# Optimization experiments

Hardware: AMD Instinct MI355X
Metric: run time of the kernel (lower is better)

Reference implementation:

```python
import jax, jax.numpy as jnp
import numpy as np

B, N, DEG = 64, 512, 16        # graphs, nodes per graph, avg degree
C, HID = 10, 128               # input feat dim (== num_classes quirk), hidden
E = B * N * DEG                # total edges (fixed; pooling masks edges)


def _gcn(x, W, b, src, dst, emask, n):
    # PyG GCNConv: add self-loops, symmetric norm D^-1/2 (A+I) D^-1/2 (XW) + b
    h = x @ W
    deg = jax.ops.segment_sum(emask, dst, num_segments=n) + 1.0  # +1 self-loop
    dinv = jax.lax.rsqrt(deg)
    norm = dinv[src] * dinv[dst] * emask
    agg = jax.ops.segment_sum(h[src] * norm[:, None], dst, num_segments=n)
    return agg + h * (dinv * dinv)[:, None] + b  # self-loop term + bias


def _sag_pool(x, src, dst, emask, Wp, bp, n_per):
    # SAGPooling: score = tanh(GCN(x)); per-graph top-k (ratio=0.5); x' = x[perm]*score
    n = x.shape[0]
    score = jnp.tanh(_gcn(x, Wp, bp, src, dst, emask, n)[:, 0])
    k = n_per // 2
    vals, idx = jax.lax.top_k(score.reshape(B, n_per), k)  # [B,k]
    perm = (idx + (jnp.arange(B) * n_per)[:, None]).reshape(-1)
    xk = x[perm] * vals.reshape(-1)[:, None]
    # relabel edges; drop edges touching removed nodes via mask (fixed E)
    mapping = jnp.full((n,), -1, jnp.int32).at[perm].set(
        jnp.arange(B * k, dtype=jnp.int32))
    ns, nd = mapping[src], mapping[dst]
    nmask = emask * ((ns >= 0) & (nd >= 0)).astype(emask.dtype)
    return xk, jnp.maximum(ns, 0), jnp.maximum(nd, 0), nmask, k


def _readout(x, k):
    # global max pool || global mean pool (all kept nodes are real, no padding)
    xg = x.reshape(B, k, -1)
    return jnp.concatenate([xg.max(axis=1), xg.mean(axis=1)], axis=1)


def setup_inputs() -> dict:
    key = jax.random.key(0)
    ks = jax.random.split(key, 16)
    x = jax.random.normal(ks[0], (B * N, C), jnp.float32)
    off = jnp.repeat(jnp.arange(B, dtype=jnp.int32) * N, N * DEG)
    src = jax.random.randint(ks[1], (E,), 0, N, jnp.int32) + off
    dst = jax.random.randint(ks[2], (E,), 0, N, jnp.int32) + off
    p = lambda k, s: jax.random.normal(k, s, jnp.float32) * 0.05
    return {
        "x": x, "src": src, "dst": dst,
        "W1": p(ks[3], (C, HID)), "b1": jnp.zeros((HID,), jnp.float32),
        "W2": p(ks[4], (HID, HID)), "b2": jnp.zeros((HID,), jnp.float32),
        "W3": p(ks[5], (HID, HID)), "b3": jnp.zeros((HID,), jnp.float32),
        "Wp": p(ks[6], (HID, 1)), "bp": jnp.zeros((1,), jnp.float32),
        "L1W": p(ks[7], (2 * HID, HID)), "L1b": jnp.zeros((HID,), jnp.float32),
        "L2W": p(ks[8], (HID, HID // 2)), "L2b": jnp.zeros((HID // 2,), jnp.float32),
    }


def reference(x, src, dst, W1, b1, W2, b2, W3, b3, Wp, bp, L1W, L1b, L2W, L2b):
    emask = jnp.ones((E,), jnp.float32)
    h = jax.nn.relu(_gcn(x, W1, b1, src, dst, emask, B * N))
    h, src, dst, emask, k = _sag_pool(h, src, dst, emask, Wp, bp, N)
    x1 = _readout(h, k)
    h = jax.nn.relu(_gcn(h, W2, b2, src, dst, emask, B * k))
    h, src, dst, emask, k = _sag_pool(h, src, dst, emask, Wp, bp, k)
    x2 = _readout(h, k)
    h = jax.nn.relu(_gcn(h, W3, b3, src, dst, emask, B * k))
    h, src, dst, emask, k = _sag_pool(h, src, dst, emask, Wp, bp, k)
    x3 = _readout(h, k)
    z = x1 + x2 + x3
    z = jax.nn.relu(z @ L1W + L1b)
    # dropout inactive in eval mode
    z = jax.nn.relu(z @ L2W + L2b)
    return jax.nn.log_softmax(z, axis=1)
```

## Files before the change

### kernel.cpp

```cpp
#include <hip/hip_runtime.h>
#include <math.h>

#define BGR 64
#define N0 512
#define E_TOT (BGR*N0*16)
#define EPG 8192
#define EIT 16
#define HID 128
#define LOFF2 32768
#define LOFF3 49152

#define HSW(r,l) (((r)<<3) | (((l)+(r))&7))

__device__ __forceinline__ void bitonic_sort(float* sv, int* si, float v, int idx,
                                             int t, int nper, bool act){
  for (int kk = 2; kk <= nper; kk <<= 1){
    for (int jj = kk >> 1; jj > 0; jj >>= 1){
      if (jj >= 64){
        if (act){ sv[t] = v; si[t] = idx; }
        __syncthreads();
        if (act){
          int p = t ^ jj;
          float pv = sv[p]; int pi = si[p];
          bool amLower = (t & jj) == 0;
          bool dirDesc = (t & kk) == 0;
          bool betterMine = (v > pv) || (v == pv && idx < pi);
          if ((amLower == dirDesc) != betterMine){ v = pv; idx = pi; }
        }
        __syncthreads();
      } else if (act){
        float pv = __shfl_xor(v, jj);
        int   pi = __shfl_xor(idx, jj);
        bool amLower = (t & jj) == 0;
        bool dirDesc = (t & kk) == 0;
        bool betterMine = (v > pv) || (v == pv && idx < pi);
        if ((amLower == dirDesc) != betterMine){ v = pv; idx = pi; }
      }
    }
  }
  if (act){ sv[t] = v; si[t] = idx; }
  __syncthreads();
}

__device__ __forceinline__ void relabel_pre(
    int2* __restrict__ edges, int2* __restrict__ csr, const int* si,
    int* map_, int* sb, int* cur, float* dl, int* wsum,
    int* __restrict__ rowptr, int* __restrict__ cnt, float* __restrict__ dinv,
    const int2* epre,
    int t, int nper, int k, int gbase, int gbnew, int ebase, int loff){
  if (t < nper) map_[t] = -1;
  if (t < k) sb[t] = 0;
  __syncthreads();
  if (t < k) map_[si[t]] = t;
  __syncthreads();
  int2 ebuf[8];
  #pragma unroll
  for (int it = 0; it < 8; it++){
    int2 e = epre[it];
    int2 ne = make_int2(-1, 0);
    if (e.x >= 0){
      int ns = map_[e.x - gbase], nd = map_[e.y - gbase];
      if (ns >= 0 && nd >= 0){
        ne = make_int2(gbnew + ns, gbnew + nd);
        atomicAdd(&sb[nd], 1);
      }
    }
    ebuf[it] = ne;
    edges[ebase + it*1024 + t] = ne;
  }
  __syncthreads();
  int vdeg = (t < k) ? sb[t] : 0;
  int lane = t & 63, wid = t >> 6;
  int x = vdeg;
  #pragma unroll
  for (int off = 1; off < 64; off <<= 1){
    int y = __shfl_up(x, off);
    if (lane >= off) x += y;
  }
  if (t < k && lane == 63) wsum[wid] = x;
  __syncthreads();
  if (t < k){
    int prefix = 0;
    #pragma unroll
    for (int wj = 0; wj < 4; wj++) prefix += (wj < wid) ? wsum[wj] : 0;
    int excl = x + prefix - vdeg;
    rowptr[loff + gbnew + t] = ebase + excl;
    cnt[loff + gbnew + t] = vdeg;
    cur[t] = excl;
    float dv = rsqrtf((float)vdeg + 1.f);
    dl[t] = dv;
    dinv[loff + gbnew + t] = dv;
  }
  __syncthreads();
  #pragma unroll
  for (int it = 0; it < 8; it++){
    int2 e = ebuf[it];
    if (e.x >= 0){
      int sl = e.x - gbnew, dc = e.y - gbnew;
      int pos = atomicAdd(&cur[dc], 1);
      csr[ebase + pos] = make_int2(e.x, __float_as_int(dl[sl]*dl[dc]));
    }
  }
  __syncthreads();
}

__global__ __launch_bounds__(512) void k_topo0(
    const int* __restrict__ s0, const int* __restrict__ d0,
    int2* __restrict__ edges, int* __restrict__ cnt, int* __restrict__ rowptr,
    float* __restrict__ dinv, int2* __restrict__ csr){
  __shared__ int   deg[512];
  __shared__ int   cur[512];
  __shared__ float dl[512];
  __shared__ int   wsum[8];
  int g = (blockIdx.x & 7)*8 + (blockIdx.x >> 3);
  int t = threadIdx.x;
  int gbase = g*N0, ebase = g*EPG;
  deg[t] = 0;
  __syncthreads();
  int2 ebuf[EIT];
  #pragma unroll
  for (int it = 0; it < EIT; it++){
    int i = ebase + it*512 + t;
    int2 e = make_int2(s0[i], d0[i]);
    ebuf[it] = e;
    edges[i] = e;
    atomicAdd(&deg[e.y - gbase], 1);
  }
  __syncthreads();
  int vdeg = deg[t];
  int lane = t & 63, wid = t >> 6;
  int x = vdeg;
  #pragma unroll
  for (int off = 1; off < 64; off <<= 1){
    int y = __shfl_up(x, off);
    if (lane >= off) x += y;
  }
  if (lane == 63) wsum[wid] = x;
  __syncthreads();
  int prefix = 0;
  #pragma unroll
  for (int wj = 0; wj < 8; wj++) prefix += (wj < wid) ? wsum[wj] : 0;
  int excl = x + prefix - vdeg;
  rowptr[gbase + t] = ebase + excl;
  cnt[gbase + t] = vdeg;
  cur[t] = excl;
  float dv = rsqrtf((float)vdeg + 1.f);
  dl[t] = dv;
  dinv[gbase + t] = dv;
  __syncthreads();
  #pragma unroll
  for (int it = 0; it < EIT; it++){
    int2 e = ebuf[it];
    int sl = e.x - gbase, dc = e.y - gbase;
    int pos = atomicAdd(&cur[dc], 1);
    csr[ebase + pos] = make_int2(e.x, __float_as_int(dl[sl]*dl[dc]));
  }
}

__global__ __launch_bounds__(512) void k_l1_fused(
    const float* __restrict__ x, const float* __restrict__ W1,
    const int2* __restrict__ csr, const int* __restrict__ rowptr,
    const int* __restrict__ cnt, const float* __restrict__ dinv,
    const float* __restrict__ b1, const float* __restrict__ Wp,
    float4* __restrict__ gout4, float* __restrict__ hp_part){
  extern __shared__ float hl[];
  int b = blockIdx.x;
  int xcd = b & 7, idx = b >> 3;
  int graph = xcd*8 + (idx >> 3);
  int sub = idx & 7;
  int qf = sub >> 1, half = sub & 1;
  int t = threadIdx.x;
  int gbase = graph*N0;
  int fp = t & 31;
  int f = qf*32 + fp;
  float wcol[10];
  #pragma unroll
  for (int k = 0; k < 10; k++) wcol[k] = W1[k*HID + f];
  for (int n = t >> 5; n < N0; n += 16){
    const float* xr = x + (gbase + n)*10;
    float acc = 0.f;
    #pragma unroll
    for (int k = 0; k < 10; k++) acc += xr[k]*wcol[k];
    hl[n*32 + ((((fp>>2)+n)&7)<<2) + (fp&3)] = acc;
  }
  __syncthreads();
  const float4* hl4 = (const float4*)hl;
  int l = t & 7, grp = t >> 3;
  float4 bb = ((const float4*)b1)[qf*8 + l];
  float4 wp = ((const float4*)Wp)[qf*8 + l];
  int n0 = half*256;
  for (int nl = n0 + grp; nl < n0 + 256; nl += 64){
    int node = gbase + nl;
    int start = rowptr[node], c = cnt[node];
    float4 acc = make_float4(0.f,0.f,0.f,0.f);
    int j = 0;
    for (; j + 4 <= c; j += 4){
      int2 e0 = csr[start+j],   e1 = csr[start+j+1];
      int2 e2 = csr[start+j+2], e3 = csr[start+j+3];
      float4 h0 = hl4[HSW(e0.x - gbase, l)];
      float4 h1 = hl4[HSW(e1.x - gbase, l)];
      float4 h2 = hl4[HSW(e2.x - gbase, l)];
      float4 h3 = hl4[HSW(e3.x - gbase, l)];
      float w0 = __int_as_float(e0.y), w1 = __int_as_float(e1.y);
      float w2 = __int_as_float(e2.y), w3 = __int_as_float(e3.y);
      acc.x += w0*h0.x + w1*h1.x + w2*h2.x + w3*h3.x;
      acc.y += w0*h0.y + w1*h1.y + w2*h2.y + w3*h3.y;
      acc.z += w0*h0.z + w1*h1.z + w2*h2.z + w3*h3.z;
      acc.w += w0*h0.w + w1*h1.w + w2*h2.w + w3*h3.w;
    }
    for (; j < c; j++){
      int2 e = csr[start + j];
      float wgt = __int_as_float(e.y);
      float4 hv = hl4[HSW(e.x - gbase, l)];
      acc.x += wgt*hv.x; acc.y += wgt*hv.y; acc.z += wgt*hv.z; acc.w += wgt*hv.w;
    }
    float di = dinv[node], dd = di*di;
    float4 hs = hl4[HSW(nl, l)];
    float4 v;
    v.x = fmaxf(acc.x + hs.x*dd + bb.x, 0.f);
    v.y = fmaxf(acc.y + hs.y*dd + bb.y, 0.f);
    v.z = fmaxf(acc.z + hs.z*dd + bb.z, 0.f);
    v.w = fmaxf(acc.w + hs.w*dd + bb.w, 0.f);
    gout4[node*32 + qf*8 + l] = v;
    float contrib = v.x*wp.x + v.y*wp.y + v.z*wp.z + v.w*wp.w;
    #pragma unroll
    for (int off = 4; off; off >>= 1) contrib += __shfl_down(contrib, off, 8);
    if (l == 0) hp_part[qf*32768 + node] = contrib;
  }
}

__global__ __launch_bounds__(1024) void k_mega1(
    const float4* __restrict__ gout4, const float* __restrict__ hppt,
    int2* __restrict__ csr, int* __restrict__ rowptr, int* __restrict__ cnt,
    float* __restrict__ dinv, const float* __restrict__ bp,
    int2* __restrict__ edges, int* __restrict__ sig, float* __restrict__ svg,
    float* __restrict__ z){
  __shared__ float sv[512];
  __shared__ int   si[512];
  __shared__ float hpl[512];
  __shared__ union UA {
    float spart[1024];
    struct { float4 pmx[16][32]; float4 psm[16][32]; } ro;
    struct { int map_[512]; int sb[512]; int cur[256]; } rl;
  } u;
  __shared__ float dl[256];
  __shared__ int   wsum[4];
  int g = (blockIdx.x & 7)*8 + (blockIdx.x >> 3);
  int t = threadIdx.x;
  int gbase = g*N0, ebase = g*EPG, gb2 = g*256;
  float bp0 = bp[0];
  int2 epre[8];
  #pragma unroll
  for (int it = 0; it < 8; it++) epre[it] = edges[ebase + it*1024 + t];
  if (t < 512){
    int node = gbase + t;
    hpl[t] = hppt[node] + hppt[32768+node] + hppt[65536+node] + hppt[98304+node];
  }
  __syncthreads();
  {
    int n = t & 511, p = t >> 9;
    int start = rowptr[gbase + n], c = cnt[gbase + n];
    int lo = (c*p) >> 1, hi = (c*(p+1)) >> 1;
    float a = 0.f;
    for (int j = lo; j < hi; j++){
      int2 e = csr[start + j];
      a += __int_as_float(e.y)*hpl[e.x - gbase];
    }
    u.spart[t] = a;
  }
  __syncthreads();
  float v = 0.f; int idx = t;
  if (t < 512){
    float a = u.spart[t] + u.spart[t + 512];
    float di = dinv[gbase + t];
    v = tanhf(a + hpl[t]*di*di + bp0);
  }
  __syncthreads();
  bitonic_sort(sv, si, v, idx, t, 512, t < 512);
  if (t < 256){ sig[g*512 + t] = si[t]; svg[g*512 + t] = sv[t]; }
  int l = t & 31, j0 = t >> 5;
  if (t < 512){
    float4 mx = make_float4(-INFINITY,-INFINITY,-INFINITY,-INFINITY);
    float4 sm = make_float4(0.f,0.f,0.f,0.f);
    for (int j = j0; j < 256; j += 16){
      float val = sv[j]; int row = si[j];
      float4 hv = gout4[(gbase + row)*32 + l];
      float4 o = make_float4(hv.x*val, hv.y*val, hv.z*val, hv.w*val);
      mx.x = fmaxf(mx.x, o.x); mx.y = fmaxf(mx.y, o.y);
      mx.z = fmaxf(mx.z, o.z); mx.w = fmaxf(mx.w, o.w);
      sm.x += o.x; sm.y += o.y; sm.z += o.z; sm.w += o.w;
    }
    u.ro.pmx[j0][l] = mx; u.ro.psm[j0][l] = sm;
  }
  __syncthreads();
  if (t < 32){
    float4 M = u.ro.pmx[0][t], S = u.ro.psm[0][t];
    #pragma unroll
    for (int q = 1; q < 16; q++){
      float4 m2 = u.ro.pmx[q][t], s2 = u.ro.psm[q][t];
      M.x = fmaxf(M.x, m2.x); M.y = fmaxf(M.y, m2.y);
      M.z = fmaxf(M.z, m2.z); M.w = fmaxf(M.w, m2.w);
      S.x += s2.x; S.y += s2.y; S.z += s2.z; S.w += s2.w;
    }
    float ki = 1.f/256.f;
    float* zp = z + g*256;
    zp[t*4+0] = M.x; zp[t*4+1] = M.y; zp[t*4+2] = M.z; zp[t*4+3] = M.w;
    zp[128+t*4+0] = S.x*ki; zp[128+t*4+1] = S.y*ki;
    zp[128+t*4+2] = S.z*ki; zp[128+t*4+3] = S.w*ki;
  }
  __syncthreads();
  relabel_pre(edges, csr, si, u.rl.map_, u.rl.sb, u.rl.cur, dl, wsum,
              rowptr, cnt, dinv, epre, t, 512, 256, gbase, gb2, ebase, LOFF2);
}

__global__ __launch_bounds__(512) void k_lvl2(
    const float4* __restrict__ gout4,
    const int* __restrict__ sig, const float* __restrict__ svg,
    const float* __restrict__ W2, const float* __restrict__ b2,
    const float* __restrict__ Wp,
    const int2* __restrict__ csr, const int* __restrict__ rowptr,
    const int* __restrict__ cnt, const float* __restrict__ dinv,
    float4* __restrict__ g2out4, float* __restrict__ hp2p){
  __shared__ float hL[256*32];
  int b = blockIdx.x;
  int jb = b & 63, s = b >> 6;
  int g = (jb & 7)*8 + (jb >> 3);
  int t = threadIdx.x;
  int gbase = g*N0, gb2 = g*256;
  float4* hL4 = (float4*)hL;
  {
    int f4 = t & 7, rg = t >> 3;
    int rbase = rg*4;
    const float* Wb = W2 + s*32 + f4*4;
    int ri[4]; float rv[4];
    #pragma unroll
    for (int q = 0; q < 4; q++){
      ri[q] = sig[g*512 + rbase + q];
      rv[q] = svg[g*512 + rbase + q];
    }
    float4 acc[4];
    #pragma unroll
    for (int q = 0; q < 4; q++) acc[q] = make_float4(0.f,0.f,0.f,0.f);
    for (int i = 0; i < HID; i += 4){
      float4 w0 = *(const float4*)(Wb + (i+0)*HID);
      float4 w1 = *(const float4*)(Wb + (i+1)*HID);
      float4 w2 = *(const float4*)(Wb + (i+2)*HID);
      float4 w3 = *(const float4*)(Wb + (i+3)*HID);
      #pragma unroll
      for (int q = 0; q < 4; q++){
        float4 xv = gout4[(gbase + ri[q])*32 + (i>>2)];
        float vx = xv.x*rv[q], vy = xv.y*rv[q], vz = xv.z*rv[q], vw = xv.w*rv[q];
        acc[q].x += vx*w0.x + vy*w1.x + vz*w2.x + vw*w3.x;
        acc[q].y += vx*w0.y + vy*w1.y + vz*w2.y + vw*w3.y;
        acc[q].z += vx*w0.z + vy*w1.z + vz*w2.z + vw*w3.z;
        acc[q].w += vx*w0.w + vy*w1.w + vz*w2.w + vw*w3.w;
      }
    }
    #pragma unroll
    for (int q = 0; q < 4; q++) hL4[HSW(rbase+q, f4)] = acc[q];
  }
  __syncthreads();
  int l = t & 7, grpn = t >> 3;
  float4 bb = ((const float4*)b2)[s*8 + l];
  float4 wp = ((const float4*)Wp)[s*8 + l];
  for (int it = 0; it < 4; it++){
    int n = it*64 + grpn;
    int node = gb2 + n;
    int start = rowptr[LOFF2 + node], c = cnt[LOFF2 + node];
    float4 acc = make_float4(0.f,0.f,0.f,0.f);
    int j = 0;
    for (; j + 4 <= c; j += 4){
      int2 e0 = csr[start+j],   e1 = csr[start+j+1];
      int2 e2 = csr[start+j+2], e3 = csr[start+j+3];
      float4 h0 = hL4[HSW(e0.x - gb2, l)];
      float4 h1 = hL4[HSW(e1.x - gb2, l)];
      float4 h2 = hL4[HSW(e2.x - gb2, l)];
      float4 h3 = hL4[HSW(e3.x - gb2, l)];
      float w0 = __int_as_float(e0.y), w1 = __int_as_float(e1.y);
      float w2 = __int_as_float(e2.y), w3 = __int_as_float(e3.y);
      acc.x += w0*h0.x + w1*h1.x + w2*h2.x + w3*h3.x;
      acc.y += w0*h0.y + w1*h1.y + w2*h2.y + w3*h3.y;
      acc.z += w0*h0.z + w1*h1.z + w2*h2.z + w3*h3.z;
      acc.w += w0*h0.w + w1*h1.w + w2*h2.w + w3*h3.w;
    }
    for (; j < c; j++){
      int2 e = csr[start + j];
      float wgt = __int_as_float(e.y);
      float4 hv = hL4[HSW(e.x - gb2, l)];
      acc.x += wgt*hv.x; acc.y += wgt*hv.y; acc.z += wgt*hv.z; acc.w += wgt*hv.w;
    }
    float di = dinv[LOFF2 + node], dd = di*di;
    float4 hs = hL4[HSW(n, l)];
    float4 v;
    v.x = fmaxf(acc.x + hs.x*dd + bb.x, 0.f);
    v.y = fmaxf(acc.y + hs.y*dd + bb.y, 0.f);
    v.z = fmaxf(acc.z + hs.z*dd + bb.z, 0.f);
    v.w = fmaxf(acc.w + hs.w*dd + bb.w, 0.f);
    g2out4[node*32 + s*8 + l] = v;
    float contrib = v.x*wp.x + v.y*wp.y + v.z*wp.z + v.w*wp.w;
    #pragma unroll
    for (int off = 4; off; off >>= 1) contrib += __shfl_down(contrib, off, 8);
    if (l == 0) hp2p[s*16384 + node] = contrib;
  }
}

__global__ __launch_bounds__(1024) void k_mega2(
    const float4* __restrict__ g2out4, const float* __restrict__ hp2p,
    int2* __restrict__ csr, int* __restrict__ rowptr, int* __restrict__ cnt,
    float* __restrict__ dinv, const float* __restrict__ bp,
    int2* __restrict__ edges, int* __restrict__ sig, float* __restrict__ svg,
    float* __restrict__ z){
  __shared__ float sv[256];
  __shared__ int   si[256];
  __shared__ float hpl[256];
  __shared__ union UB {
    float spart[1024];
    struct { float4 pmx[16][32]; float4 psm[16][32]; } ro;
    struct { int map_[256]; int sb[128]; int cur[128]; } rl;
  } u;
  __shared__ float dl[128];
  __shared__ int   wsum[4];
  int g = (blockIdx.x & 7)*8 + (blockIdx.x >> 3);
  int t = threadIdx.x;
  int gb2 = g*256, gb3 = g*128, ebase = g*EPG;
  float bp0 = bp[0];
  int2 epre[8];
  #pragma unroll
  for (int it = 0; it < 8; it++) epre[it] = edges[ebase + it*1024 + t];
  if (t < 256){
    int node = gb2 + t;
    hpl[t] = hp2p[node] + hp2p[16384+node] + hp2p[32768+node] + hp2p[49152+node];
  }
  __syncthreads();
  {
    int n = t & 255, p = t >> 8;
    int start = rowptr[LOFF2 + gb2 + n], c = cnt[LOFF2 + gb2 + n];
    int lo = (c*p) >> 2, hi = (c*(p+1)) >> 2;
    float a = 0.f;
    for (int j = lo; j < hi; j++){
      int2 e = csr[start + j];
      a += __int_as_float(e.y)*hpl[e.x - gb2];
    }
    u.spart[t] = a;
  }
  __syncthreads();
  float v = 0.f; int idx = t;
  if (t < 256){
    float a = u.spart[t] + u.spart[t+256] + u.spart[t+512] + u.spart[t+768];
    float di = dinv[LOFF2 + gb2 + t];
    v = tanhf(a + hpl[t]*di*di + bp0);
  }
  __syncthreads();
  bitonic_sort(sv, si, v, idx, t, 256, t < 256);
  if (t < 128){ sig[g*512 + t] = si[t]; svg[g*512 + t] = sv[t]; }
  int l = t & 31, j0 = t >> 5;
  if (t < 512){
    float4 mx = make_float4(-INFINITY,-INFINITY,-INFINITY,-INFINITY);
    float4 sm = make_float4(0.f,0.f,0.f,0.f);
    for (int j = j0; j < 128; j += 16){
      float val = sv[j]; int row = si[j];
      float4 hv = g2out4[(gb2 + row)*32 + l];
      float4 o = make_float4(hv.x*val, hv.y*val, hv.z*val, hv.w*val);
      mx.x = fmaxf(mx.x, o.x); mx.y = fmaxf(mx.y, o.y);
      mx.z = fmaxf(mx.z, o.z); mx.w = fmaxf(mx.w, o.w);
      sm.x += o.x; sm.y += o.y; sm.z += o.z; sm.w += o.w;
    }
    u.ro.pmx[j0][l] = mx; u.ro.psm[j0][l] = sm;
  }
  __syncthreads();
  if (t < 32){
    float4 M = u.ro.pmx[0][t], S = u.ro.psm[0][t];
    #pragma unroll
    for (int q = 1; q < 16; q++){
      float4 m2 = u.ro.pmx[q][t], s2 = u.ro.psm[q][t];
      M.x = fmaxf(M.x, m2.x); M.y = fmaxf(M.y, m2.y);
      M.z = fmaxf(M.z, m2.z); M.w = fmaxf(M.w, m2.w);
      S.x += s2.x; S.y += s2.y; S.z += s2.z; S.w += s2.w;
    }
    float ki = 1.f/128.f;
    float* zp = z + g*256;
    zp[t*4+0] += M.x; zp[t*4+1] += M.y; zp[t*4+2] += M.z; zp[t*4+3] += M.w;
    zp[128+t*4+0] += S.x*ki; zp[128+t*4+1] += S.y*ki;
    zp[128+t*4+2] += S.z*ki; zp[128+t*4+3] += S.w*ki;
  }
  __syncthreads();
  relabel_pre(edges, csr, si, u.rl.map_, u.rl.sb, u.rl.cur, dl, wsum,
              rowptr, cnt, dinv, epre, t, 256, 128, gb2, gb3, ebase, LOFF3);
}

__global__ __launch_bounds__(512) void k_lvl3(
    const float4* __restrict__ g2out4,
    const int* __restrict__ sig, const float* __restrict__ svg,
    const float* __restrict__ W3, const float* __restrict__ b3,
    const float* __restrict__ Wp,
    const int2* __restrict__ csr, const int* __restrict__ rowptr,
    const int* __restrict__ cnt, const float* __restrict__ dinv,
    float4* __restrict__ g3out4, float* __restrict__ hp3p){
  __shared__ float hL[128*32];
  int b = blockIdx.x;
  int jb = b & 63, s = b >> 6;
  int g = (jb & 7)*8 + (jb >> 3);
  int t = threadIdx.x;
  int gb2 = g*256, gb3 = g*128;
  float4* hL4 = (float4*)hL;
  {
    int f4 = t & 7, rg = t >> 3;
    int rbase = rg*2;
    const float* Wb = W3 + s*32 + f4*4;
    int ri[2]; float rv[2];
    #pragma unroll
    for (int q = 0; q < 2; q++){
      ri[q] = sig[g*512 + rbase + q];
      rv[q] = svg[g*512 + rbase + q];
    }
    float4 acc[2];
    #pragma unroll
    for (int q = 0; q < 2; q++) acc[q] = make_float4(0.f,0.f,0.f,0.f);
    for (int i = 0; i < HID; i += 4){
      float4 w0 = *(const float4*)(Wb + (i+0)*HID);
      float4 w1 = *(const float4*)(Wb + (i+1)*HID);
      float4 w2 = *(const float4*)(Wb + (i+2)*HID);
      float4 w3 = *(const float4*)(Wb + (i+3)*HID);
      #pragma unroll
      for (int q = 0; q < 2; q++){
        float4 xv = g2out4[(gb2 + ri[q])*32 + (i>>2)];
        float vx = xv.x*rv[q], vy = xv.y*rv[q], vz = xv.z*rv[q], vw = xv.w*rv[q];
        acc[q].x += vx*w0.x + vy*w1.x + vz*w2.x + vw*w3.x;
        acc[q].y += vx*w0.y + vy*w1.y + vz*w2.y + vw*w3.y;
        acc[q].z += vx*w0.z + vy*w1.z + vz*w2.z + vw*w3.z;
        acc[q].w += vx*w0.w + vy*w1.w + vz*w2.w + vw*w3.w;
      }
    }
    #pragma unroll
    for (int q = 0; q < 2; q++) hL4[HSW(rbase+q, f4)] = acc[q];
  }
  __syncthreads();
  int l = t & 7, grpn = t >> 3;
  float4 bb = ((const float4*)b3)[s*8 + l];
  float4 wp = ((const float4*)Wp)[s*8 + l];
  for (int it = 0; it < 2; it++){
    int n = it*64 + grpn;
    int node = gb3 + n;
    int start = rowptr[LOFF3 + node], c = cnt[LOFF3 + node];
    float4 acc = make_float4(0.f,0.f,0.f,0.f);
    int j = 0;
    for (; j + 4 <= c; j += 4){
      int2 e0 = csr[start+j],   e1 = csr[start+j+1];
      int2 e2 = csr[start+j+2], e3 = csr[start+j+3];
      float4 h0 = hL4[HSW(e0.x - gb3, l)];
      float4 h1 = hL4[HSW(e1.x - gb3, l)];
      float4 h2 = hL4[HSW(e2.x - gb3, l)];
      float4 h3 = hL4[HSW(e3.x - gb3, l)];
      float w0 = __int_as_float(e0.y), w1 = __int_as_float(e1.y);
      float w2 = __int_as_float(e2.y), w3 = __int_as_float(e3.y);
      acc.x += w0*h0.x + w1*h1.x + w2*h2.x + w3*h3.x;
      acc.y += w0*h0.y + w1*h1.y + w2*h2.y + w3*h3.y;
      acc.z += w0*h0.z + w1*h1.z + w2*h2.z + w3*h3.z;
      acc.w += w0*h0.w + w1*h1.w + w2*h2.w + w3*h3.w;
    }
    for (; j < c; j++){
      int2 e = csr[start + j];
      float wgt = __int_as_float(e.y);
      float4 hv = hL4[HSW(e.x - gb3, l)];
      acc.x += wgt*hv.x; acc.y += wgt*hv.y; acc.z += wgt*hv.z; acc.w += wgt*hv.w;
    }
    float di = dinv[LOFF3 + node], dd = di*di;
    float4 hs = hL4[HSW(n, l)];
    float4 v;
    v.x = fmaxf(acc.x + hs.x*dd + bb.x, 0.f);
    v.y = fmaxf(acc.y + hs.y*dd + bb.y, 0.f);
    v.z = fmaxf(acc.z + hs.z*dd + bb.z, 0.f);
    v.w = fmaxf(acc.w + hs.w*dd + bb.w, 0.f);
    g3out4[node*32 + s*8 + l] = v;
    float contrib = v.x*wp.x + v.y*wp.y + v.z*wp.z + v.w*wp.w;
    #pragma unroll
    for (int off = 4; off; off >>= 1) contrib += __shfl_down(contrib, off, 8);
    if (l == 0) hp3p[s*8192 + node] = contrib;
  }
}

__global__ __launch_bounds__(1024) void k_mega3(
    const float4* __restrict__ g3out4, const float* __restrict__ hp3p,
    const int2* __restrict__ csr, const int* __restrict__ rowptr,
    const int* __restrict__ cnt, const float* __restrict__ dinv,
    const float* __restrict__ bp, float* __restrict__ z,
    const float* __restrict__ L1W, const float* __restrict__ L1b,
    const float* __restrict__ L2W, const float* __restrict__ L2b,
    float* __restrict__ out){
  __shared__ float sv[128];
  __shared__ int   si[128];
  __shared__ float hpl[128];
  __shared__ union UC {
    float spart[1024];
    struct { float4 pmx[16][32]; float4 psm[16][32]; } ro;
  } u;
  __shared__ float zr[256];
  __shared__ float h1l[128];
  __shared__ float h2l[64];
  __shared__ float red[2];
  int g = (blockIdx.x & 7)*8 + (blockIdx.x >> 3);
  int t = threadIdx.x;
  int gb3 = g*128;
  float bp0 = bp[0];
  if (t < 128){
    int node = gb3 + t;
    hpl[t] = hp3p[node] + hp3p[8192+node] + hp3p[16384+node] + hp3p[24576+node];
  }
  __syncthreads();
  {
    int n = t & 127, p = t >> 7;
    int start = rowptr[LOFF3 + gb3 + n], c = cnt[LOFF3 + gb3 + n];
    int lo = (c*p) >> 3, hi = (c*(p+1)) >> 3;
    float a = 0.f;
    for (int j = lo; j < hi; j++){
      int2 e = csr[start + j];
      a += __int_as_float(e.y)*hpl[e.x - gb3];
    }
    u.spart[t] = a;
  }
  __syncthreads();
  float v = 0.f; int idx = t;
  if (t < 128){
    float a = 0.f;
    #pragma unroll
    for (int pp = 0; pp < 8; pp++) a += u.spart[t + pp*128];
    float di = dinv[LOFF3 + gb3 + t];
    v = tanhf(a + hpl[t]*di*di + bp0);
  }
  __syncthreads();
  bitonic_sort(sv, si, v, idx, t, 128, t < 128);
  int l = t & 31, j0 = t >> 5;
  if (t < 512){
    float4 mx = make_float4(-INFINITY,-INFINITY,-INFINITY,-INFINITY);
    float4 sm = make_float4(0.f,0.f,0.f,0.f);
    for (int j = j0; j < 64; j += 16){
      float val = sv[j]; int row = si[j];
      float4 hv = g3out4[(gb3 + row)*32 + l];
      float4 o = make_float4(hv.x*val, hv.y*val, hv.z*val, hv.w*val);
      mx.x = fmaxf(mx.x, o.x); mx.y = fmaxf(mx.y, o.y);
      mx.z = fmaxf(mx.z, o.z); mx.w = fmaxf(mx.w, o.w);
      sm.x += o.x; sm.y += o.y; sm.z += o.z; sm.w += o.w;
    }
    u.ro.pmx[j0][l] = mx; u.ro.psm[j0][l] = sm;
  }
  __syncthreads();
  if (t < 32){
    float4 M = u.ro.pmx[0][t], S = u.ro.psm[0][t];
    #pragma unroll
    for (int q = 1; q < 16; q++){
      float4 m2 = u.ro.pmx[q][t], s2 = u.ro.psm[q][t];
      M.x = fmaxf(M.x, m2.x); M.y = fmaxf(M.y, m2.y);
      M.z = fmaxf(M.z, m2.z); M.w = fmaxf(M.w, m2.w);
      S.x += s2.x; S.y += s2.y; S.z += s2.z; S.w += s2.w;
    }
    float ki = 1.f/64.f;
    float* zp = z + g*256;
    zr[t*4+0] = zp[t*4+0] + M.x; zr[t*4+1] = zp[t*4+1] + M.y;
    zr[t*4+2] = zp[t*4+2] + M.z; zr[t*4+3] = zp[t*4+3] + M.w;
    zr[128+t*4+0] = zp[128+t*4+0] + S.x*ki;
    zr[128+t*4+1] = zp[128+t*4+1] + S.y*ki;
    zr[128+t*4+2] = zp[128+t*4+2] + S.z*ki;
    zr[128+t*4+3] = zp[128+t*4+3] + S.w*ki;
  }
  __syncthreads();
  if (t < 128){
    float a = L1b[t];
    for (int i = 0; i < 256; i++) a += zr[i]*L1W[i*128 + t];
    h1l[t] = fmaxf(a, 0.f);
  }
  __syncthreads();
  if (t < 64){
    float a = L2b[t];
    for (int i = 0; i < 128; i++) a += h1l[i]*L2W[i*64 + t];
    h2l[t] = fmaxf(a, 0.f);
  }
  __syncthreads();
  if (t == 0){
    float mxv = -INFINITY;
    for (int i = 0; i < 64; i++) mxv = fmaxf(mxv, h2l[i]);
    float s = 0.f;
    for (int i = 0; i < 64; i++) s += expf(h2l[i] - mxv);
    red[0] = mxv; red[1] = logf(s);
  }
  __syncthreads();
  if (t < 64) out[g*64 + t] = h2l[t] - red[0] - red[1];
}

extern "C" void kernel_launch(void* const* d_in, const int* in_sizes, int n_in,
                              void* d_out, int out_size, void* d_ws, size_t ws_size,
                              hipStream_t stream){
  (void)in_sizes; (void)n_in; (void)out_size; (void)ws_size;
  const float* x0  = (const float*)d_in[0];
  const int*   s0  = (const int*)  d_in[1];
  const int*   d0  = (const int*)  d_in[2];
  const float* W1  = (const float*)d_in[3];  const float* b1 = (const float*)d_in[4];
  const float* W2  = (const float*)d_in[5];  const float* b2 = (const float*)d_in[6];
  const float* W3  = (const float*)d_in[7];  const float* b3 = (const float*)d_in[8];
  const float* Wp  = (const float*)d_in[9];  const float* bp = (const float*)d_in[10];
  const float* L1W = (const float*)d_in[11]; const float* L1b = (const float*)d_in[12];
  const float* L2W = (const float*)d_in[13]; const float* L2b = (const float*)d_in[14];
  float* out = (float*)d_out;

  float* w = (float*)d_ws;
  float* gout1 = w; w += 32768*HID;
  float* gout2 = w; w += 16384*HID;
  float* gout3 = w; w += 8192*HID;
  float* dinvv = w; w += 65536;
  float* hppt  = w; w += 4*32768;
  float* hp2p  = w; w += 4*16384;
  float* hp3p  = w; w += 4*8192;
  float* z     = w; w += BGR*256;
  float* svg   = w; w += 32768;
  int* sig     = (int*)w; w += 32768;
  int* cnt     = (int*)w; w += 65536;
  int* rowptr  = (int*)w; w += 65536;
  int2* edges  = (int2*)w; w += 2*E_TOT;
  int2* csr    = (int2*)w; w += 2*E_TOT;

  k_topo0<<<BGR, 512, 0, stream>>>(s0, d0, edges, cnt, rowptr, dinvv, csr);
  k_l1_fused<<<512, 512, 65536, stream>>>(x0, W1, csr, rowptr, cnt, dinvv,
                                          b1, Wp, (float4*)gout1, hppt);
  k_mega1<<<BGR, 1024, 0, stream>>>((const float4*)gout1, hppt, csr, rowptr,
                                    cnt, dinvv, bp, edges, sig, svg, z);
  k_lvl2<<<4*BGR, 512, 0, stream>>>((const float4*)gout1, sig, svg, W2, b2, Wp,
                                    csr, rowptr, cnt, dinvv,
                                    (float4*)gout2, hp2p);
  k_mega2<<<BGR, 1024, 0, stream>>>((const float4*)gout2, hp2p, csr, rowptr,
                                    cnt, dinvv, bp, edges, sig, svg, z);
  k_lvl3<<<4*BGR, 512, 0, stream>>>((const float4*)gout2, sig, svg, W3, b3, Wp,
                                    csr, rowptr, cnt, dinvv,
                                    (float4*)gout3, hp3p);
  k_mega3<<<BGR, 1024, 0, stream>>>((const float4*)gout3, hp3p, csr, rowptr,
                                    cnt, dinvv, bp, z,
                                    L1W, L1b, L2W, L2b, out);
}
```

Before: 233.6 us.

## Fuse level-2 pooling, level-3 GCN and final readout into one per-graph kernel

Merges k_mega2, k_lvl3 and k_mega3 into a single kernel with one 1024-thread block per graph. Level-3 features, the relabelled CSR (packed as 16-bit shorts) and the degree norms stay in LDS, so the global round trips and two launches go away. The level-3 GCN output is recomputed for the top-k rows during readout instead of being stored. The cost is a much larger LDS footprint (a 64KB h3 plus a 16KB csr buffer), only 64 blocks doing the W3 matmul that was previously spread over 256 blocks, and less parallelism in the tail.

Result: slower. 247.7 us (+6.0%).

```diff
diff --git a/kernel.cpp b/kernel.cpp
--- a/kernel.cpp
+++ b/kernel.cpp
@@ -8,7 +8,6 @@
 #define EIT 16
 #define HID 128
 #define LOFF2 32768
-#define LOFF3 49152
 
 #define HSW(r,l) (((r)<<3) | (((l)+(r))&7))
 
@@ -404,32 +403,51 @@
   }
 }
 
-__global__ __launch_bounds__(1024) void k_mega2(
+__global__ __launch_bounds__(1024) void k_tail23(
     const float4* __restrict__ g2out4, const float* __restrict__ hp2p,
-    int2* __restrict__ csr, int* __restrict__ rowptr, int* __restrict__ cnt,
-    float* __restrict__ dinv, const float* __restrict__ bp,
-    int2* __restrict__ edges, int* __restrict__ sig, float* __restrict__ svg,
-    float* __restrict__ z){
+    const int2* __restrict__ csr, const int* __restrict__ rowptr,
+    const int* __restrict__ cnt, const float* __restrict__ dinv,
+    const float* __restrict__ bp, const int2* __restrict__ edges,
+    const float* __restrict__ W3, const float* __restrict__ b3,
+    const float* __restrict__ Wp, const float* __restrict__ z,
+    const float* __restrict__ L1W, const float* __restrict__ L1b,
+    const float* __restrict__ L2W, const float* __restrict__ L2b,
+    float* __restrict__ out){
   __shared__ float sv[256];
   __shared__ int   si[256];
   __shared__ float hpl[256];
-  __shared__ union UB {
+  __shared__ float zacc[256];
+  __shared__ union UT {
     float spart[1024];
     struct { float4 pmx[16][32]; float4 psm[16][32]; } ro;
-    struct { int map_[256]; int sb[128]; int cur[128]; } rl;
+    struct { float4 pmx[32][32]; float4 psm[32][32]; } ro3;
+    struct { int map_[256]; int sb[128]; } rl;
   } u;
-  __shared__ float dl[128];
-  __shared__ int   wsum[4];
+  __shared__ int   cur[128];
+  __shared__ float dl3[128];
+  __shared__ int   rpl[128];
+  __shared__ int   cnt3[128];
+  __shared__ int   wsum[2];
+  __shared__ unsigned short csr3s[EPG];
+  __shared__ float h3[128*HID];
+  __shared__ float h1l[128];
+  __shared__ float h2l[64];
+  __shared__ float red[2];
+
   int g = (blockIdx.x & 7)*8 + (blockIdx.x >> 3);
   int t = threadIdx.x;
-  int gb2 = g*256, gb3 = g*128, ebase = g*EPG;
+  int gb2 = g*256, ebase = g*EPG;
+  int l = t & 31, j0 = t >> 5;
   float bp0 = bp[0];
+  const float4* h34 = (const float4*)h3;
+
   int2 epre[8];
   #pragma unroll
   for (int it = 0; it < 8; it++) epre[it] = edges[ebase + it*1024 + t];
   if (t < 256){
     int node = gb2 + t;
     hpl[t] = hp2p[node] + hp2p[16384+node] + hp2p[32768+node] + hp2p[49152+node];
+    zacc[t] = z[g*256 + t];
   }
   __syncthreads();
   {
@@ -452,8 +470,6 @@
   }
   __syncthreads();
   bitonic_sort(sv, si, v, idx, t, 256, t < 256);
-  if (t < 128){ sig[g*512 + t] = si[t]; svg[g*512 + t] = sv[t]; }
-  int l = t & 31, j0 = t >> 5;
   if (t < 512){
     float4 mx = make_float4(-INFINITY,-INFINITY,-INFINITY,-INFINITY);
     float4 sm = make_float4(0.f,0.f,0.f,0.f);
@@ -478,51 +494,77 @@
       S.x += s2.x; S.y += s2.y; S.z += s2.z; S.w += s2.w;
     }
     float ki = 1.f/128.f;
-    float* zp = z + g*256;
-    zp[t*4+0] += M.x; zp[t*4+1] += M.y; zp[t*4+2] += M.z; zp[t*4+3] += M.w;
-    zp[128+t*4+0] += S.x*ki; zp[128+t*4+1] += S.y*ki;
-    zp[128+t*4+2] += S.z*ki; zp[128+t*4+3] += S.w*ki;
-  }
-  __syncthreads();
-  relabel_pre(edges, csr, si, u.rl.map_, u.rl.sb, u.rl.cur, dl, wsum,
-              rowptr, cnt, dinv, epre, t, 256, 128, gb2, gb3, ebase, LOFF3);
-}
-
-__global__ __launch_bounds__(512) void k_lvl3(
-    const float4* __restrict__ g2out4,
-    const int* __restrict__ sig, const float* __restrict__ svg,
-    const float* __restrict__ W3, const float* __restrict__ b3,
-    const float* __restrict__ Wp,
-    const int2* __restrict__ csr, const int* __restrict__ rowptr,
-    const int* __restrict__ cnt, const float* __restrict__ dinv,
-    float4* __restrict__ g3out4, float* __restrict__ hp3p){
-  __shared__ float hL[128*32];
-  int b = blockIdx.x;
-  int jb = b & 63, s = b >> 6;
-  int g = (jb & 7)*8 + (jb >> 3);
-  int t = threadIdx.x;
-  int gb2 = g*256, gb3 = g*128;
-  float4* hL4 = (float4*)hL;
+    zacc[t*4+0] += M.x; zacc[t*4+1] += M.y; zacc[t*4+2] += M.z; zacc[t*4+3] += M.w;
+    zacc[128+t*4+0] += S.x*ki; zacc[128+t*4+1] += S.y*ki;
+    zacc[128+t*4+2] += S.z*ki; zacc[128+t*4+3] += S.w*ki;
+  }
+  __syncthreads();
+  if (t < 256) u.rl.map_[t] = -1;
+  if (t < 128) u.rl.sb[t] = 0;
+  __syncthreads();
+  if (t < 128) u.rl.map_[si[t]] = t;
+  __syncthreads();
+  int2 ebuf[8];
+  #pragma unroll
+  for (int it = 0; it < 8; it++){
+    int2 e = epre[it];
+    int2 ne = make_int2(-1, 0);
+    if (e.x >= 0){
+      int ns = u.rl.map_[e.x - gb2], nd = u.rl.map_[e.y - gb2];
+      if (ns >= 0 && nd >= 0){
+        ne = make_int2(ns, nd);
+        atomicAdd(&u.rl.sb[nd], 1);
+      }
+    }
+    ebuf[it] = ne;
+  }
+  __syncthreads();
   {
-    int f4 = t & 7, rg = t >> 3;
-    int rbase = rg*2;
-    const float* Wb = W3 + s*32 + f4*4;
-    int ri[2]; float rv[2];
-    #pragma unroll
-    for (int q = 0; q < 2; q++){
-      ri[q] = sig[g*512 + rbase + q];
-      rv[q] = svg[g*512 + rbase + q];
-    }
-    float4 acc[2];
-    #pragma unroll
-    for (int q = 0; q < 2; q++) acc[q] = make_float4(0.f,0.f,0.f,0.f);
+    int vdeg = (t < 128) ? u.rl.sb[t] : 0;
+    int lane = t & 63, wid = t >> 6;
+    int x = vdeg;
+    #pragma unroll
+    for (int off = 1; off < 64; off <<= 1){
+      int y = __shfl_up(x, off);
+      if (lane >= off) x += y;
+    }
+    if (t < 128 && lane == 63) wsum[wid] = x;
+    __syncthreads();
+    if (t < 128){
+      int excl = x + ((wid == 1) ? wsum[0] : 0) - vdeg;
+      rpl[t] = excl;
+      cnt3[t] = vdeg;
+      cur[t] = excl;
+      dl3[t] = rsqrtf((float)vdeg + 1.f);
+    }
+  }
+  __syncthreads();
+  #pragma unroll
+  for (int it = 0; it < 8; it++){
+    int2 e = ebuf[it];
+    if (e.x >= 0){
+      int pos = atomicAdd(&cur[e.y], 1);
+      csr3s[pos] = (unsigned short)((e.y << 8) | e.x);
+    }
+  }
+  __syncthreads();
+  {
+    int f4 = t & 31, rg = t >> 5;
+    int rbase = rg*4;
+    const float* Wb = W3 + f4*4;
+    int ri[4]; float rv[4];
+    #pragma unroll
+    for (int q = 0; q < 4; q++){ ri[q] = si[rbase+q]; rv[q] = sv[rbase+q]; }
+    float4 acc[4];
+    #pragma unroll
+    for (int q = 0; q < 4; q++) acc[q] = make_float4(0.f,0.f,0.f,0.f);
     for (int i = 0; i < HID; i += 4){
       float4 w0 = *(const float4*)(Wb + (i+0)*HID);
       float4 w1 = *(const float4*)(Wb + (i+1)*HID);
       float4 w2 = *(const float4*)(Wb + (i+2)*HID);
       float4 w3 = *(const float4*)(Wb + (i+3)*HID);
       #pragma unroll
-      for (int q = 0; q < 2; q++){
+      for (int q = 0; q < 4; q++){
         float4 xv = g2out4[(gb2 + ri[q])*32 + (i>>2)];
         float vx = xv.x*rv[q], vy = xv.y*rv[q], vz = xv.z*rv[q], vw = xv.w*rv[q];
         acc[q].x += vx*w0.x + vy*w1.x + vz*w2.x + vw*w3.x;
@@ -532,140 +574,110 @@
       }
     }
     #pragma unroll
-    for (int q = 0; q < 2; q++) hL4[HSW(rbase+q, f4)] = acc[q];
-  }
-  __syncthreads();
-  int l = t & 7, grpn = t >> 3;
-  float4 bb = ((const float4*)b3)[s*8 + l];
-  float4 wp = ((const float4*)Wp)[s*8 + l];
-  for (int it = 0; it < 2; it++){
-    int n = it*64 + grpn;
-    int node = gb3 + n;
-    int start = rowptr[LOFF3 + node], c = cnt[LOFF3 + node];
-    float4 acc = make_float4(0.f,0.f,0.f,0.f);
-    int j = 0;
-    for (; j + 4 <= c; j += 4){
-      int2 e0 = csr[start+j],   e1 = csr[start+j+1];
-      int2 e2 = csr[start+j+2], e3 = csr[start+j+3];
-      float4 h0 = hL4[HSW(e0.x - gb3, l)];
-      float4 h1 = hL4[HSW(e1.x - gb3, l)];
-      float4 h2 = hL4[HSW(e2.x - gb3, l)];
-      float4 h3 = hL4[HSW(e3.x - gb3, l)];
-      float w0 = __int_as_float(e0.y), w1 = __int_as_float(e1.y);
-      float w2 = __int_as_float(e2.y), w3 = __int_as_float(e3.y);
-      acc.x += w0*h0.x + w1*h1.x + w2*h2.x + w3*h3.x;
-      acc.y += w0*h0.y + w1*h1.y + w2*h2.y + w3*h3.y;
-      acc.z += w0*h0.z + w1*h1.z + w2*h2.z + w3*h3.z;
-      acc.w += w0*h0.w + w1*h1.w + w2*h2.w + w3*h3.w;
-    }
-    for (; j < c; j++){
-      int2 e = csr[start + j];
-      float wgt = __int_as_float(e.y);
-      float4 hv = hL4[HSW(e.x - gb3, l)];
-      acc.x += wgt*hv.x; acc.y += wgt*hv.y; acc.z += wgt*hv.z; acc.w += wgt*hv.w;
-    }
-    float di = dinv[LOFF3 + node], dd = di*di;
-    float4 hs = hL4[HSW(n, l)];
-    float4 v;
-    v.x = fmaxf(acc.x + hs.x*dd + bb.x, 0.f);
-    v.y = fmaxf(acc.y + hs.y*dd + bb.y, 0.f);
-    v.z = fmaxf(acc.z + hs.z*dd + bb.z, 0.f);
-    v.w = fmaxf(acc.w + hs.w*dd + bb.w, 0.f);
-    g3out4[node*32 + s*8 + l] = v;
-    float contrib = v.x*wp.x + v.y*wp.y + v.z*wp.z + v.w*wp.w;
-    #pragma unroll
-    for (int off = 4; off; off >>= 1) contrib += __shfl_down(contrib, off, 8);
-    if (l == 0) hp3p[s*8192 + node] = contrib;
-  }
-}
-
-__global__ __launch_bounds__(1024) void k_mega3(
-    const float4* __restrict__ g3out4, const float* __restrict__ hp3p,
-    const int2* __restrict__ csr, const int* __restrict__ rowptr,
-    const int* __restrict__ cnt, const float* __restrict__ dinv,
-    const float* __restrict__ bp, float* __restrict__ z,
-    const float* __restrict__ L1W, const float* __restrict__ L1b,
-    const float* __restrict__ L2W, const float* __restrict__ L2b,
-    float* __restrict__ out){
-  __shared__ float sv[128];
-  __shared__ int   si[128];
-  __shared__ float hpl[128];
-  __shared__ union UC {
-    float spart[1024];
-    struct { float4 pmx[16][32]; float4 psm[16][32]; } ro;
-  } u;
-  __shared__ float zr[256];
-  __shared__ float h1l[128];
-  __shared__ float h2l[64];
-  __shared__ float red[2];
-  int g = (blockIdx.x & 7)*8 + (blockIdx.x >> 3);
-  int t = threadIdx.x;
-  int gb3 = g*128;
-  float bp0 = bp[0];
-  if (t < 128){
-    int node = gb3 + t;
-    hpl[t] = hp3p[node] + hp3p[8192+node] + hp3p[16384+node] + hp3p[24576+node];
+    for (int q = 0; q < 4; q++)
+      *((float4*)h3 + (rbase+q)*32 + f4) = acc[q];
+  }
+  __syncthreads();
+  {
+    float4 bb = ((const float4*)b3)[l];
+    float4 wp4 = ((const float4*)Wp)[l];
+    for (int it = 0; it < 4; it++){
+      int n = it*32 + j0;
+      float dln = dl3[n];
+      int start = rpl[n], c = cnt3[n];
+      float4 acc = make_float4(0.f,0.f,0.f,0.f);
+      for (int j = 0; j < c; j++){
+        int src = csr3s[start + j] & 255;
+        float w = dl3[src]*dln;
+        float4 hv = h34[src*32 + l];
+        acc.x += w*hv.x; acc.y += w*hv.y; acc.z += w*hv.z; acc.w += w*hv.w;
+      }
+      float dd = dln*dln;
+      float4 hs = h34[n*32 + l];
+      float4 vv;
+      vv.x = fmaxf(acc.x + hs.x*dd + bb.x, 0.f);
+      vv.y = fmaxf(acc.y + hs.y*dd + bb.y, 0.f);
+      vv.z = fmaxf(acc.z + hs.z*dd + bb.z, 0.f);
+      vv.w = fmaxf(acc.w + hs.w*dd + bb.w, 0.f);
+      float contrib = vv.x*wp4.x + vv.y*wp4.y + vv.z*wp4.z + vv.w*wp4.w;
+      #pragma unroll
+      for (int off = 16; off; off >>= 1) contrib += __shfl_down(contrib, off, 32);
+      if (l == 0) hpl[n] = contrib;
+    }
   }
   __syncthreads();
   {
     int n = t & 127, p = t >> 7;
-    int start = rowptr[LOFF3 + gb3 + n], c = cnt[LOFF3 + gb3 + n];
+    int start = rpl[n], c = cnt3[n];
     int lo = (c*p) >> 3, hi = (c*(p+1)) >> 3;
+    float dln = dl3[n];
     float a = 0.f;
     for (int j = lo; j < hi; j++){
-      int2 e = csr[start + j];
-      a += __int_as_float(e.y)*hpl[e.x - gb3];
+      int src = csr3s[start + j] & 255;
+      a += dl3[src]*dln*hpl[src];
     }
     u.spart[t] = a;
   }
   __syncthreads();
-  float v = 0.f; int idx = t;
+  v = 0.f; idx = t;
   if (t < 128){
     float a = 0.f;
     #pragma unroll
     for (int pp = 0; pp < 8; pp++) a += u.spart[t + pp*128];
-    float di = dinv[LOFF3 + gb3 + t];
-    v = tanhf(a + hpl[t]*di*di + bp0);
+    v = tanhf(a + hpl[t]*dl3[t]*dl3[t] + bp0);
   }
   __syncthreads();
   bitonic_sort(sv, si, v, idx, t, 128, t < 128);
-  int l = t & 31, j0 = t >> 5;
-  if (t < 512){
+  {
+    float4 bb = ((const float4*)b3)[l];
     float4 mx = make_float4(-INFINITY,-INFINITY,-INFINITY,-INFINITY);
     float4 sm = make_float4(0.f,0.f,0.f,0.f);
-    for (int j = j0; j < 64; j += 16){
+    #pragma unroll
+    for (int it = 0; it < 2; it++){
+      int j = it*32 + j0;
       float val = sv[j]; int row = si[j];
-      float4 hv = g3out4[(gb3 + row)*32 + l];
-      float4 o = make_float4(hv.x*val, hv.y*val, hv.z*val, hv.w*val);
+      float dlr = dl3[row];
+      int start = rpl[row], c = cnt3[row];
+      float4 acc = make_float4(0.f,0.f,0.f,0.f);
+      for (int jj = 0; jj < c; jj++){
+        int src = csr3s[start + jj] & 255;
+        float w = dl3[src]*dlr;
+        float4 hv = h34[src*32 + l];
+        acc.x += w*hv.x; acc.y += w*hv.y; acc.z += w*hv.z; acc.w += w*hv.w;
+      }
+      float dd = dlr*dlr;
+      float4 hs = h34[row*32 + l];
+      float4 vv;
+      vv.x = fmaxf(acc.x + hs.x*dd + bb.x, 0.f);
+      vv.y = fmaxf(acc.y + hs.y*dd + bb.y, 0.f);
+      vv.z = fmaxf(acc.z + hs.z*dd + bb.z, 0.f);
+      vv.w = fmaxf(acc.w + hs.w*dd + bb.w, 0.f);
+      float4 o = make_float4(vv.x*val, vv.y*val, vv.z*val, vv.w*val);
       mx.x = fmaxf(mx.x, o.x); mx.y = fmaxf(mx.y, o.y);
       mx.z = fmaxf(mx.z, o.z); mx.w = fmaxf(mx.w, o.w);
       sm.x += o.x; sm.y += o.y; sm.z += o.z; sm.w += o.w;
     }
-    u.ro.pmx[j0][l] = mx; u.ro.psm[j0][l] = sm;
+    u.ro3.pmx[j0][l] = mx; u.ro3.psm[j0][l] = sm;
   }
   __syncthreads();
   if (t < 32){
-    float4 M = u.ro.pmx[0][t], S = u.ro.psm[0][t];
-    #pragma unroll
-    for (int q = 1; q < 16; q++){
-      float4 m2 = u.ro.pmx[q][t], s2 = u.ro.psm[q][t];
+    float4 M = u.ro3.pmx[0][t], S = u.ro3.psm[0][t];
+    #pragma unroll
+    for (int q = 1; q < 32; q++){
+      float4 m2 = u.ro3.pmx[q][t], s2 = u.ro3.psm[q][t];
       M.x = fmaxf(M.x, m2.x); M.y = fmaxf(M.y, m2.y);
       M.z = fmaxf(M.z, m2.z); M.w = fmaxf(M.w, m2.w);
       S.x += s2.x; S.y += s2.y; S.z += s2.z; S.w += s2.w;
     }
     float ki = 1.f/64.f;
-    float* zp = z + g*256;
-    zr[t*4+0] = zp[t*4+0] + M.x; zr[t*4+1] = zp[t*4+1] + M.y;
-    zr[t*4+2] = zp[t*4+2] + M.z; zr[t*4+3] = zp[t*4+3] + M.w;
-    zr[128+t*4+0] = zp[128+t*4+0] + S.x*ki;
-    zr[128+t*4+1] = zp[128+t*4+1] + S.y*ki;
-    zr[128+t*4+2] = zp[128+t*4+2] + S.z*ki;
-    zr[128+t*4+3] = zp[128+t*4+3] + S.w*ki;
+    zacc[t*4+0] += M.x; zacc[t*4+1] += M.y; zacc[t*4+2] += M.z; zacc[t*4+3] += M.w;
+    zacc[128+t*4+0] += S.x*ki; zacc[128+t*4+1] += S.y*ki;
+    zacc[128+t*4+2] += S.z*ki; zacc[128+t*4+3] += S.w*ki;
   }
   __syncthreads();
   if (t < 128){
     float a = L1b[t];
-    for (int i = 0; i < 256; i++) a += zr[i]*L1W[i*128 + t];
+    for (int i = 0; i < 256; i++) a += zacc[i]*L1W[i*128 + t];
     h1l[t] = fmaxf(a, 0.f);
   }
   __syncthreads();
@@ -704,11 +716,9 @@
   float* w = (float*)d_ws;
   float* gout1 = w; w += 32768*HID;
   float* gout2 = w; w += 16384*HID;
-  float* gout3 = w; w += 8192*HID;
   float* dinvv = w; w += 65536;
   float* hppt  = w; w += 4*32768;
   float* hp2p  = w; w += 4*16384;
-  float* hp3p  = w; w += 4*8192;
   float* z     = w; w += BGR*256;
   float* svg   = w; w += 32768;
   int* sig     = (int*)w; w += 32768;
@@ -725,12 +735,7 @@
   k_lvl2<<<4*BGR, 512, 0, stream>>>((const float4*)gout1, sig, svg, W2, b2, Wp,
                                     csr, rowptr, cnt, dinvv,
                                     (float4*)gout2, hp2p);
-  k_mega2<<<BGR, 1024, 0, stream>>>((const float4*)gout2, hp2p, csr, rowptr,
-                                    cnt, dinvv, bp, edges, sig, svg, z);
-  k_lvl3<<<4*BGR, 512, 0, stream>>>((const float4*)gout2, sig, svg, W3, b3, Wp,
-                                    csr, rowptr, cnt, dinvv,
-                                    (float4*)gout3, hp3p);
-  k_mega3<<<BGR, 1024, 0, stream>>>((const float4*)gout3, hp3p, csr, rowptr,
-                                    cnt, dinvv, bp, z,
-                                    L1W, L1b, L2W, L2b, out);
+  k_tail23<<<BGR, 1024, 0, stream>>>((const float4*)gout2, hp2p, csr, rowptr,
+                                     cnt, dinvv, bp, edges, W3, b3, Wp, z,
+                                     L1W, L1b, L2W, L2b, out);
 }
```
